# Kernel optimization log

Hardware: AMD Instinct MI355X
Metric: run time of the kernel (lower is better)

Reference implementation:

```python
import jax, jax.numpy as jnp
import numpy as np

H = 16          # num_heads
W = 256         # sliding window size
LN_EPS = 1e-6
ROPE_BASE = 10000.0


def layer_norm(x, g, b):
    m = jnp.mean(x, axis=-1, keepdims=True)
    v = jnp.mean((x - m) ** 2, axis=-1, keepdims=True)
    return (x - m) * jax.lax.rsqrt(v + LN_EPS) * g + b


def rope(x):
    # x: [B, S, H, hd]; rotate-half RoPE
    S, hd = x.shape[1], x.shape[-1]
    inv_freq = 1.0 / (ROPE_BASE ** (jnp.arange(0, hd, 2, dtype=jnp.float32) / hd))
    ang = jnp.arange(S, dtype=jnp.float32)[:, None] * inv_freq[None, :]  # [S, hd/2]
    cos = jnp.concatenate([jnp.cos(ang), jnp.cos(ang)], axis=-1)[None, :, None, :]
    sin = jnp.concatenate([jnp.sin(ang), jnp.sin(ang)], axis=-1)[None, :, None, :]
    x1, x2 = jnp.split(x, 2, axis=-1)
    rot = jnp.concatenate([-x2, x1], axis=-1)
    return x * cos + rot * sin


def setup_inputs() -> dict:
    key = jax.random.key(0)
    ks = jax.random.split(key, 12)
    B, S, D, I = 2, 2048, 1024, 4096
    s = 0.02
    return {
        "hidden_states": jax.random.normal(ks[0], (B, S, D), jnp.float32),
        "wq": jax.random.normal(ks[1], (D, D), jnp.float32) * s,
        "wk": jax.random.normal(ks[2], (D, D), jnp.float32) * s,
        "wv": jax.random.normal(ks[3], (D, D), jnp.float32) * s,
        "wo": jax.random.normal(ks[4], (D, D), jnp.float32) * s,
        "w1": jax.random.normal(ks[5], (D, I), jnp.float32) * s,
        "w2": jax.random.normal(ks[6], (I, D), jnp.float32) * s,
        "w3": jax.random.normal(ks[7], (D, I), jnp.float32) * s,
        "ln1_g": jnp.ones((D,), jnp.float32),
        "ln1_b": jnp.zeros((D,), jnp.float32),
        "ln2_g": jnp.ones((D,), jnp.float32),
        "ln2_b": jnp.zeros((D,), jnp.float32),
    }


def reference(hidden_states, wq, wk, wv, wo, w1, w2, w3, ln1_g, ln1_b, ln2_g, ln2_b):
    B, S, D = hidden_states.shape
    hd = D // H

    # --- attention sub-block ---
    residual = hidden_states
    x = layer_norm(hidden_states, ln1_g, ln1_b)
    q = (x @ wq).reshape(B, S, H, hd)
    k = (x @ wk).reshape(B, S, H, hd)
    v = (x @ wv).reshape(B, S, H, hd)
    q, k = rope(q), rope(k)

    scores = jnp.einsum("bqhd,bkhd->bhqk", q, k) / jnp.sqrt(jnp.float32(hd))
    idx = jnp.arange(S)
    rel = idx[:, None] - idx[None, :]          # i - j
    mask = (rel >= 0) & (rel < W)              # causal sliding window
    scores = jnp.where(mask[None, None], scores, jnp.float32(-1e9))
    attn = jax.nn.softmax(scores, axis=-1)
    ctx = jnp.einsum("bhqk,bkhd->bqhd", attn, v).reshape(B, S, D)
    hidden_states = residual + ctx @ wo

    # --- SwiGLU MLP sub-block ---
    residual = hidden_states
    x = layer_norm(hidden_states, ln2_g, ln2_b)
    mlp = (jax.nn.silu(x @ w1) * (x @ w3)) @ w2
    return residual + mlp
```

## Files before the change

kernel.cpp:

```cpp
#include <hip/hip_runtime.h>
#include <hip/hip_bf16.h>

typedef __bf16 bf16_t;
typedef __bf16 bf16x4 __attribute__((ext_vector_type(4)));
typedef __bf16 bf16x8 __attribute__((ext_vector_type(8)));
typedef float f32x4 __attribute__((ext_vector_type(4)));

#define LN_EPS 1e-6f

__device__ __forceinline__ void gl2lds16(const void* g, void* l) {
    __builtin_amdgcn_global_load_lds(
        (const __attribute__((address_space(1))) void*)g,
        (__attribute__((address_space(3))) void*)l, 16, 0, 0);
}

__device__ __forceinline__ void block_sync() {
    __asm__ __volatile__("" ::: "memory");
    __builtin_amdgcn_s_barrier();
    __asm__ __volatile__("" ::: "memory");
}

__device__ __forceinline__ void ln_row(const float* __restrict__ x, const float* __restrict__ g,
                                       const float* __restrict__ bb, bf16_t* __restrict__ out,
                                       int row, int t, float* sbuf, float* sbuf2) {
    const int D = 1024;
    const float4* xr = reinterpret_cast<const float4*>(x + (size_t)row * D);
    float4 v = xr[t];
    float s = v.x + v.y + v.z + v.w;
    int wave = t >> 6, lane = t & 63;
#pragma unroll
    for (int o = 32; o > 0; o >>= 1) s += __shfl_xor(s, o);
    if (lane == 0) sbuf[wave] = s;
    __syncthreads();
    float mean = (sbuf[0] + sbuf[1] + sbuf[2] + sbuf[3]) / (float)D;
    float d0 = v.x - mean, d1 = v.y - mean, d2 = v.z - mean, d3 = v.w - mean;
    float sq = d0 * d0 + d1 * d1 + d2 * d2 + d3 * d3;
#pragma unroll
    for (int o = 32; o > 0; o >>= 1) sq += __shfl_xor(sq, o);
    if (lane == 0) sbuf2[wave] = sq;
    __syncthreads();
    float var = (sbuf2[0] + sbuf2[1] + sbuf2[2] + sbuf2[3]) / (float)D;
    float inv = rsqrtf(var + LN_EPS);
    float4 gv = reinterpret_cast<const float4*>(g)[t];
    float4 bv = reinterpret_cast<const float4*>(bb)[t];
    bf16x4 o4;
    o4[0] = (bf16_t)(d0 * inv * gv.x + bv.x);
    o4[1] = (bf16_t)(d1 * inv * gv.y + bv.y);
    o4[2] = (bf16_t)(d2 * inv * gv.z + bv.z);
    o4[3] = (bf16_t)(d3 * inv * gv.w + bv.w);
    *reinterpret_cast<bf16x4*>(out + (size_t)row * D + t * 4) = o4;
}

__global__ void prep_weights_kernel(const float* __restrict__ wq, const float* __restrict__ wk,
                                    const float* __restrict__ wv, const float* __restrict__ wo,
                                    const float* __restrict__ w1, const float* __restrict__ w3,
                                    const float* __restrict__ w2, bf16_t* __restrict__ wq_t,
                                    bf16_t* __restrict__ wk_t, bf16_t* __restrict__ wv_t,
                                    bf16_t* __restrict__ wo_t, bf16_t* __restrict__ w13_t,
                                    bf16_t* __restrict__ w2_t, const float* __restrict__ hs,
                                    const float* __restrict__ ln1g, const float* __restrict__ ln1b,
                                    bf16_t* __restrict__ x_b) {
    __shared__ float tile[32][33];
    __shared__ float sbuf[4];
    __shared__ float sbuf2[4];
    int id = blockIdx.x;
    if (id >= 16384) {
        ln_row(hs, ln1g, ln1b, x_b, id - 16384, threadIdx.x, sbuf, sbuf2);
        return;
    }
    const float* src;
    bf16_t* dst;
    int R, C, mode = 0;
    if (id < 4096) {
        int w = id >> 10;
        id &= 1023;
        src = (w == 0) ? wq : (w == 1) ? wk : (w == 2) ? wv : wo;
        dst = (w == 0) ? wq_t : (w == 1) ? wk_t : (w == 2) ? wv_t : wo_t;
        R = 1024; C = 1024;
    } else if (id < 8192) {
        id -= 4096; src = w1; dst = w13_t; R = 1024; C = 4096; mode = 1;
    } else if (id < 12288) {
        id -= 8192; src = w3; dst = w13_t; R = 1024; C = 4096; mode = 2;
    } else {
        id -= 12288; src = w2; dst = w2_t; R = 4096; C = 1024;
    }
    int tpc = C >> 5;
    int bx = id % tpc, by = id / tpc;
    int r0 = by * 32, c0 = bx * 32;
    int tx = threadIdx.x & 31;
    int ty = threadIdx.x >> 5;
#pragma unroll
    for (int i = 0; i < 4; i++) {
        int r = ty + i * 8;
        tile[r][tx] = src[(size_t)(r0 + r) * C + (c0 + tx)];
    }
    __syncthreads();
#pragma unroll
    for (int i = 0; i < 4; i++) {
        int r = ty + i * 8;
        int rr = c0 + r;
        if (mode) rr = ((rr >> 7) << 8) + (rr & 127) + ((mode == 2) ? 128 : 0);
        dst[(size_t)rr * R + (r0 + tx)] = (bf16_t)tile[tx][r];
    }
}

__global__ void ln_kernel(const float* __restrict__ x, const float* __restrict__ g,
                          const float* __restrict__ bb, bf16_t* __restrict__ out, int D) {
    __shared__ float sbuf[4];
    __shared__ float sbuf2[4];
    ln_row(x, g, bb, out, blockIdx.x, threadIdx.x, sbuf, sbuf2);
}

#define G4_BK 64

template <int EPI>
__launch_bounds__(256, 2) __global__
void gemm4_kernel(const bf16_t* __restrict__ A, const bf16_t* __restrict__ Bt,
                  float* __restrict__ Cf, const float* __restrict__ aux,
                  const bf16_t* __restrict__ auxb, bf16_t* __restrict__ Cb,
                  int M, int N, int K, int lda, int ldb) {
    __shared__ __align__(16) bf16_t As[128 * G4_BK];
    __shared__ __align__(16) bf16_t Bs[128 * G4_BK];
    const int t = threadIdx.x;
    const int wave = t >> 6, lane = t & 63;
    const int lr = lane & 15, quad = lane >> 4;
    const int wm = (wave >> 1) * 64, wn = (wave & 1) * 64;

    const int gx = gridDim.x, gy = gridDim.y;
    const int nwg = gx * gy;
    const int lin = blockIdx.y * gx + blockIdx.x;
    const int qch = nwg >> 3;
    const int sw = (lin & 7) * qch + (lin >> 3);
    const int m0 = (sw / gy) * 128;
    const int n0 = (sw % gy) * 128;
    const int koff = blockIdx.z * K;

    const int srow = t >> 3;
    const int sslot = (t & 7) ^ (srow & 7);
    const bf16_t* agp = A + (size_t)(m0 + srow) * lda + koff + sslot * 8;
    const bf16_t* bgp = Bt + (size_t)(n0 + srow) * ldb + koff + sslot * 8;
    bf16_t* asl = As + t * 8;
    bf16_t* bsl = Bs + t * 8;

    int aoff[4][2], boff[4][2];
#pragma unroll
    for (int f = 0; f < 4; f++)
#pragma unroll
        for (int s = 0; s < 2; s++) {
            int ra = wm + f * 16 + lr;
            int rb = wn + f * 16 + lr;
            aoff[f][s] = ra * G4_BK + (((s * 4 + quad) ^ (ra & 7)) << 3);
            boff[f][s] = rb * G4_BK + (((s * 4 + quad) ^ (rb & 7)) << 3);
        }

    f32x4 acc[4][4];
#pragma unroll
    for (int mi = 0; mi < 4; mi++)
#pragma unroll
        for (int ni = 0; ni < 4; ni++) acc[mi][ni] = 0.f;

    for (int k0 = 0; k0 < K; k0 += G4_BK) {
#pragma unroll
        for (int i = 0; i < 4; i++)
            gl2lds16(agp + k0 + (size_t)(32 * i) * lda, asl + i * 2048);
#pragma unroll
        for (int i = 0; i < 4; i++)
            gl2lds16(bgp + k0 + (size_t)(32 * i) * ldb, bsl + i * 2048);
        __syncthreads();
#pragma unroll
        for (int s = 0; s < 2; s++) {
            bf16x8 af[4], bfv[4];
#pragma unroll
            for (int mi = 0; mi < 4; mi++)
                af[mi] = *reinterpret_cast<const bf16x8*>(&As[aoff[mi][s]]);
#pragma unroll
            for (int ni = 0; ni < 4; ni++)
                bfv[ni] = *reinterpret_cast<const bf16x8*>(&Bs[boff[ni][s]]);
#pragma unroll
            for (int mi = 0; mi < 4; mi++)
#pragma unroll
                for (int ni = 0; ni < 4; ni++)
                    acc[mi][ni] = __builtin_amdgcn_mfma_f32_16x16x32_bf16(af[mi], bfv[ni],
                                                                          acc[mi][ni], 0, 0, 0);
        }
        __syncthreads();
    }

#pragma unroll
    for (int mi = 0; mi < 4; mi++)
#pragma unroll
        for (int ni = 0; ni < 4; ni++)
#pragma unroll
            for (int j = 0; j < 4; j++) {
                int gm = m0 + wm + mi * 16 + quad * 4 + j;
                int gn = n0 + wn + ni * 16 + lr;
                size_t idx = (size_t)gm * N + gn;
                float val = acc[mi][ni][j];
                if constexpr (EPI == 1) {
                    Cf[idx] = val + aux[idx];
                }
            }
}


template <int QM, int QN>
__device__ __forceinline__ void quad_mfma(f32x4 (&acc)[2][2][4][2], const bf16x8 (&af)[4][2],
                                          const bf16x8 (&bf)[2][2]) {
#pragma unroll
    for (int fr = 0; fr < 4; fr++)
#pragma unroll
        for (int fc = 0; fc < 2; fc++)
#pragma unroll
            for (int ks = 0; ks < 2; ks++)
                acc[QM][QN][fr][fc] = __builtin_amdgcn_mfma_f32_16x16x32_bf16(
                    af[fr][ks], bf[fc][ks], acc[QM][QN][fr][fc], 0, 0, 0);
}

template <int EPI>
__launch_bounds__(512, 2) __global__
void gemm6_kernel(const bf16_t* __restrict__ A, const bf16_t* __restrict__ Bt,
                  const bf16_t* __restrict__ auxb, bf16_t* __restrict__ Cb,
                  bf16_t* __restrict__ Cb2, int M, int N, int K, int lda, int ldb) {
    extern __shared__ __align__(16) bf16_t smem[];
    bf16_t* smA = smem;
    bf16_t* smB = smem + 32768;
    const int t = threadIdx.x;
    const int wave = t >> 6, lane = t & 63;
    const int lr = lane & 15, quad = lane >> 4;
    const int rowgrp = wave >> 2;
    const int colgrp = wave & 3;
    const int cg1 = colgrp & 1, cg2 = colgrp >> 1;

    const int gx = gridDim.x, gy = gridDim.y;
    const int nwg = gx * gy;
    const int lin = blockIdx.y * gx + blockIdx.x;
    int m0t, n0t;
    if (gy == 32) {
        int s = lin >> 8, r = lin & 255, x = r & 7, j = r >> 3;
        m0t = s * 8 + (x & 1) * 4 + (j >> 3);
        n0t = (x >> 1) * 8 + (j & 7);
    } else if (gy == 12) {
        int x = lin & 7, j = lin >> 3;
        m0t = (x & 3) * 4 + j / 6;
        n0t = (x >> 2) * 6 + j % 6;
    } else {
        const int qch = nwg >> 3;
        const int sw = (lin & 7) * qch + (lin >> 3);
        m0t = sw / gy;
        n0t = sw % gy;
    }
    const int m0 = m0t * 256;
    const int n0 = n0t * 256;
    const int koff = blockIdx.z * K;

    const bf16_t* Ag = A + (size_t)m0 * lda + koff;
    const bf16_t* Bg = Bt + (size_t)n0 * ldb + koff;

    const int li0 = (wave * 2 + 0) * 64 + lane;
    const int li1 = (wave * 2 + 1) * 64 + lane;
    const int r0s = li0 >> 3, c0s = ((li0 & 7) ^ (r0s & 7)) << 3;
    const int r1s = li1 >> 3, c1s = ((li1 & 7) ^ (r1s & 7)) << 3;
    const bf16_t* pA0[2] = {Ag + (size_t)r0s * lda + c0s, Ag + (size_t)r1s * lda + c1s};
    const bf16_t* pA1[2] = {pA0[0] + (size_t)128 * lda, pA0[1] + (size_t)128 * lda};
    const bf16_t* pB0[2] = {Bg + (size_t)r0s * ldb + c0s, Bg + (size_t)r1s * ldb + c1s};
    const bf16_t* pB1[2] = {pB0[0] + (size_t)128 * ldb, pB0[1] + (size_t)128 * ldb};
    const int dl0 = (wave * 2 + 0) * 512;
    const int dl1 = (wave * 2 + 1) * 512;

#define STG(P, LBASE)                          \
    do {                                       \
        gl2lds16(P[0], (LBASE) + dl0);         \
        P[0] += 64;                            \
        gl2lds16(P[1], (LBASE) + dl1);         \
        P[1] += 64;                            \
    } while (0)

    int aoff[4][2], boff[2][2];
#pragma unroll
    for (int fr = 0; fr < 4; fr++)
#pragma unroll
        for (int ks = 0; ks < 2; ks++) {
            int ra = rowgrp * 64 + fr * 16 + lr;
            aoff[fr][ks] = ra * 64 + (((ks * 4 + quad) ^ (ra & 7)) << 3);
        }
#pragma unroll
    for (int fc = 0; fc < 2; fc++)
#pragma unroll
        for (int ks = 0; ks < 2; ks++) {
            int rb = cg1 * 64 + cg2 * 16 + fc * 32 + lr;
            boff[fc][ks] = rb * 64 + (((ks * 4 + quad) ^ (rb & 7)) << 3);
        }

    f32x4 acc[2][2][4][2];
#pragma unroll
    for (int qm = 0; qm < 2; qm++)
#pragma unroll
        for (int qn = 0; qn < 2; qn++)
#pragma unroll
            for (int fr = 0; fr < 4; fr++)
#pragma unroll
                for (int fc = 0; fc < 2; fc++) acc[qm][qn][fr][fc] = 0.f;

    const int NT = K >> 6;

    STG(pA0, smA);
    STG(pB0, smB);
    STG(pB1, smB + 8192);
    STG(pA1, smA + 8192);
    if (NT > 1) {
        STG(pA0, smA + 16384);
        __asm__ __volatile__("s_waitcnt vmcnt(2)" ::: "memory");
    } else {
        __asm__ __volatile__("s_waitcnt vmcnt(0)" ::: "memory");
    }
    block_sync();

    bf16x8 af[4][2], bf0[2][2], bf1[2][2];

    for (int tt = 0; tt < NT; ++tt) {
        const int cur = tt & 1, nxt = cur ^ 1;
        const bf16_t* A0b = smA + cur * 16384;
        const bf16_t* A1b = A0b + 8192;
        const bf16_t* B0b = smB + cur * 16384;
        const bf16_t* B1b = B0b + 8192;
        bf16_t* sAn = smA + nxt * 16384;
        bf16_t* sBn = smB + nxt * 16384;
        bf16_t* sAc = smA + cur * 16384;
        const bool pf1 = (tt + 1 < NT);
        const bool pf2 = (tt + 2 < NT);

#pragma unroll
        for (int fr = 0; fr < 4; fr++)
#pragma unroll
            for (int ks = 0; ks < 2; ks++)
                af[fr][ks] = *reinterpret_cast<const bf16x8*>(A0b + aoff[fr][ks]);
#pragma unroll
        for (int fc = 0; fc < 2; fc++)
#pragma unroll
            for (int ks = 0; ks < 2; ks++)
                bf0[fc][ks] = *reinterpret_cast<const bf16x8*>(B0b + boff[fc][ks]);
        if (pf1) STG(pB0, sBn);
        block_sync();
        __asm__ __volatile__("s_waitcnt lgkmcnt(0)" ::: "memory");
        __builtin_amdgcn_sched_barrier(0);
        __builtin_amdgcn_s_setprio(1);
        quad_mfma<0, 0>(acc, af, bf0);
        __builtin_amdgcn_s_setprio(0);
        block_sync();

#pragma unroll
        for (int fc = 0; fc < 2; fc++)
#pragma unroll
            for (int ks = 0; ks < 2; ks++)
                bf1[fc][ks] = *reinterpret_cast<const bf16x8*>(B1b + boff[fc][ks]);
        if (pf1) STG(pB1, sBn + 8192);
        block_sync();
        __asm__ __volatile__("s_waitcnt lgkmcnt(0)" ::: "memory");
        __builtin_amdgcn_sched_barrier(0);
        __builtin_amdgcn_s_setprio(1);
        quad_mfma<0, 1>(acc, af, bf1);
        __builtin_amdgcn_s_setprio(0);
        block_sync();

#pragma unroll
        for (int fr = 0; fr < 4; fr++)
#pragma unroll
            for (int ks = 0; ks < 2; ks++)
                af[fr][ks] = *reinterpret_cast<const bf16x8*>(A1b + aoff[fr][ks]);
        if (pf1) STG(pA1, sAn + 8192);
        block_sync();
        __asm__ __volatile__("s_waitcnt lgkmcnt(0)" ::: "memory");
        __builtin_amdgcn_sched_barrier(0);
        __builtin_amdgcn_s_setprio(1);
        quad_mfma<1, 1>(acc, af, bf1);
        __builtin_amdgcn_s_setprio(0);
        block_sync();

        if (pf2) STG(pA0, sAc);
        __builtin_amdgcn_s_setprio(1);
        quad_mfma<1, 0>(acc, af, bf0);
        __builtin_amdgcn_s_setprio(0);
        __asm__ __volatile__("s_waitcnt vmcnt(2)" ::: "memory");
        block_sync();
    }
#undef STG

    if constexpr (EPI == 3) {
        if (n0 < 2048) {
            const float kfreq = -0.41524101186f;
            const int d = cg2 * 16 + lr;
            const float freq = exp2f((float)d * kfreq);
#pragma unroll
            for (int qm = 0; qm < 2; qm++)
#pragma unroll
                for (int qn = 0; qn < 2; qn++) {
                    const int gnb = n0 + qn * 128 + cg1 * 64;
#pragma unroll
                    for (int fr = 0; fr < 4; fr++)
#pragma unroll
                        for (int j = 0; j < 4; j++) {
                            int gm = m0 + qm * 128 + rowgrp * 64 + fr * 16 + quad * 4 + j;
                            float pos = (float)(gm & 2047);
                            float ang = pos * freq;
                            float sn, cs;
                            __sincosf(ang, &sn, &cs);
                            float x1 = acc[qm][qn][fr][0][j];
                            float x2 = acc[qm][qn][fr][1][j];
                            size_t idx = (size_t)gm * N + gnb + d;
                            Cb[idx] = (bf16_t)(x1 * cs - x2 * sn);
                            Cb[idx + 32] = (bf16_t)(x2 * cs + x1 * sn);
                        }
                }
        } else {
#pragma unroll
            for (int qm = 0; qm < 2; qm++)
#pragma unroll
                for (int qn = 0; qn < 2; qn++)
#pragma unroll
                    for (int fr = 0; fr < 4; fr++)
#pragma unroll
                        for (int fc = 0; fc < 2; fc++) {
                            int gmb = m0 + qm * 128 + rowgrp * 64 + fr * 16 + quad * 4;
                            int vcol = (n0 - 2048) + qn * 128 + cg1 * 64 + cg2 * 16 + fc * 32 + lr;
                            int hh = vcol >> 6, dd = vcol & 63;
                            int bb2 = gmb >> 11, ss = gmb & 2047;
                            bf16x4 pk;
#pragma unroll
                            for (int j = 0; j < 4; j++) pk[j] = (bf16_t)acc[qm][qn][fr][fc][j];
                            *reinterpret_cast<bf16x4*>(
                                &Cb2[(((size_t)(bb2 * 16 + hh)) * 64 + dd) * 2048 + ss]) = pk;
                        }
        }
    } else if constexpr (EPI == 6) {
        const int No = N >> 1;
#pragma unroll
        for (int qm = 0; qm < 2; qm++)
#pragma unroll
            for (int fr = 0; fr < 4; fr++)
#pragma unroll
                for (int fc = 0; fc < 2; fc++)
#pragma unroll
                    for (int j = 0; j < 4; j++) {
                        int gm = m0 + qm * 128 + rowgrp * 64 + fr * 16 + quad * 4 + j;
                        int c = (n0 >> 1) + cg1 * 64 + cg2 * 16 + fc * 32 + lr;
                        float a = acc[qm][0][fr][fc][j];
                        float bv = acc[qm][1][fr][fc][j];
                        float sl = a / (1.0f + __expf(-a));
                        Cb[(size_t)gm * No + c] = (bf16_t)(sl * bv);
                    }
    } else {
        size_t outoff = (EPI == 5) ? (size_t)blockIdx.z * M * N : 0;
#pragma unroll
        for (int qm = 0; qm < 2; qm++)
#pragma unroll
            for (int qn = 0; qn < 2; qn++)
#pragma unroll
                for (int fr = 0; fr < 4; fr++)
#pragma unroll
                    for (int fc = 0; fc < 2; fc++)
#pragma unroll
                        for (int j = 0; j < 4; j++) {
                            int gm = m0 + qm * 128 + rowgrp * 64 + fr * 16 + quad * 4 + j;
                            int gn = n0 + qn * 128 + cg1 * 64 + cg2 * 16 + fc * 32 + lr;
                            size_t idx = (size_t)gm * N + gn;
                            float val = acc[qm][qn][fr][fc][j];
                            if constexpr (EPI == 5) {
                                Cb[outoff + idx] = (bf16_t)val;
                            } else {
                                Cb[idx] = (bf16_t)val;
                            }
                        }
    }
}

__global__ void reduce4_kernel(const bf16_t* __restrict__ p, const float* __restrict__ hid,
                               float* __restrict__ out, int n4) {
    int i = blockIdx.x * 256 + threadIdx.x;
    if (i >= n4) return;
    size_t i4 = (size_t)i * 4;
    float4 h = *reinterpret_cast<const float4*>(hid + i4);
    const size_t stride = (size_t)4096 * 1024;
#pragma unroll
    for (int c = 0; c < 4; c++) {
        bf16x4 a = *reinterpret_cast<const bf16x4*>(p + c * stride + i4);
        h.x += (float)a[0];
        h.y += (float)a[1];
        h.z += (float)a[2];
        h.w += (float)a[3];
    }
    *reinterpret_cast<float4*>(out + i4) = h;
}

#define PSTR 40
#define QKVS 3072
__global__ __launch_bounds__(256, 2) void attn_kernel(const bf16_t* __restrict__ qkv,
                                                      const bf16_t* __restrict__ vt,
                                                      bf16_t* __restrict__ ctx, int S) {
    __shared__ __align__(16) bf16_t Pbuf[4][16 * PSTR];
    int t = threadIdx.x;
    int wave = t >> 6, lane = t & 63;
    int col = lane & 15, quad = lane >> 4;
    int h = blockIdx.y, b = blockIdx.z;
    int q0 = blockIdx.x * 64 + wave * 16;

    const bf16_t* qrow = qkv + (size_t)(b * S + q0 + col) * QKVS + h * 64;
    bf16x8 aq0 = *reinterpret_cast<const bf16x8*>(qrow + quad * 8);
    bf16x8 aq1 = *reinterpret_cast<const bf16x8*>(qrow + 32 + quad * 8);

    int jbase = q0 - 256;
    f32x4 sc[17];
#pragma unroll
    for (int kt = 0; kt < 17; kt++) {
        int j = jbase + kt * 16 + col;
        int jc = j < 0 ? 0 : (j > S - 1 ? S - 1 : j);
        const bf16_t* krow = qkv + (size_t)(b * S + jc) * QKVS + 1024 + h * 64;
        bf16x8 bk0 = *reinterpret_cast<const bf16x8*>(krow + quad * 8);
        bf16x8 bk1 = *reinterpret_cast<const bf16x8*>(krow + 32 + quad * 8);
        f32x4 c0 = {0.f, 0.f, 0.f, 0.f};
        c0 = __builtin_amdgcn_mfma_f32_16x16x32_bf16(aq0, bk0, c0, 0, 0, 0);
        c0 = __builtin_amdgcn_mfma_f32_16x16x32_bf16(aq1, bk1, c0, 0, 0, 0);
        sc[kt] = c0;
    }
#pragma unroll
    for (int kt = 0; kt < 17; kt++) {
#pragma unroll
        for (int jj = 0; jj < 4; jj++) {
            int qq = quad * 4 + jj;
            int j = jbase + kt * 16 + col;
            int rel = (q0 + qq) - j;
            bool ok = (j >= 0) && (rel >= 0) && (rel < 256);
            sc[kt][jj] = ok ? sc[kt][jj] * 0.125f : -1e30f;
        }
    }
    float sminv[4];
#pragma unroll
    for (int jj = 0; jj < 4; jj++) {
        float m = -1e30f;
#pragma unroll
        for (int kt = 0; kt < 17; kt++) m = fmaxf(m, sc[kt][jj]);
#pragma unroll
        for (int o = 1; o < 16; o <<= 1) m = fmaxf(m, __shfl_xor(m, o));
        float s = 0.f;
#pragma unroll
        for (int kt = 0; kt < 17; kt++) {
            float p = __expf(sc[kt][jj] - m);
            sc[kt][jj] = p;
            s += p;
        }
#pragma unroll
        for (int o = 1; o < 16; o <<= 1) s += __shfl_xor(s, o);
        sminv[jj] = 1.0f / s;
    }
    f32x4 o[4];
#pragma unroll
    for (int n = 0; n < 4; n++) o[n] = 0.f;
    bf16_t* myP = Pbuf[wave];
    const bf16_t* vplane = vt + ((size_t)(b * 16 + h)) * 64 * S;
#pragma unroll
    for (int c = 0; c < 9; c++) {
#pragma unroll
        for (int half = 0; half < 2; half++) {
            int kt = 2 * c + half;
#pragma unroll
            for (int jj = 0; jj < 4; jj++) {
                int qq = quad * 4 + jj;
                bf16_t pv = (kt < 17) ? (bf16_t)(sc[kt < 17 ? kt : 0][jj] * sminv[jj])
                                      : (bf16_t)0.f;
                myP[qq * PSTR + half * 16 + col] = pv;
            }
        }
        bf16x8 ap = *reinterpret_cast<const bf16x8*>(myP + col * PSTR + quad * 8);
        int key0 = jbase + c * 32 + quad * 8;
        int kc = key0 < 0 ? 0 : (key0 > S - 8 ? S - 8 : key0);
#pragma unroll
        for (int n = 0; n < 4; n++) {
            bf16x8 bv = *reinterpret_cast<const bf16x8*>(vplane + ((size_t)(n * 16 + col)) * S + kc);
            o[n] = __builtin_amdgcn_mfma_f32_16x16x32_bf16(ap, bv, o[n], 0, 0, 0);
        }
    }
#pragma unroll
    for (int n = 0; n < 4; n++)
#pragma unroll
        for (int jj = 0; jj < 4; jj++) {
            int qq = quad * 4 + jj;
            ctx[((size_t)(b * S + q0 + qq) * 16 + h) * 64 + n * 16 + col] = (bf16_t)o[n][jj];
        }
}

extern "C" void kernel_launch(void* const* d_in, const int* in_sizes, int n_in,
                              void* d_out, int out_size, void* d_ws, size_t ws_size,
                              hipStream_t stream) {
    const float* hs   = (const float*)d_in[0];
    const float* wq   = (const float*)d_in[1];
    const float* wk   = (const float*)d_in[2];
    const float* wv   = (const float*)d_in[3];
    const float* wo   = (const float*)d_in[4];
    const float* w1   = (const float*)d_in[5];
    const float* w2   = (const float*)d_in[6];
    const float* w3   = (const float*)d_in[7];
    const float* ln1g = (const float*)d_in[8];
    const float* ln1b = (const float*)d_in[9];
    const float* ln2g = (const float*)d_in[10];
    const float* ln2b = (const float*)d_in[11];
    float* out = (float*)d_out;

    const int B = 2, S = 2048, D = 1024, I = 4096;
    const int BS = B * S;

    char* ws = (char*)d_ws;
    const size_t MB = 1024 * 1024;
    bf16_t* wq_t  = (bf16_t*)(ws + 0 * MB);
    bf16_t* wk_t  = (bf16_t*)(ws + 2 * MB);
    bf16_t* wv_t  = (bf16_t*)(ws + 4 * MB);
    bf16_t* wo_t  = (bf16_t*)(ws + 6 * MB);
    bf16_t* w13_t = (bf16_t*)(ws + 8 * MB);
    bf16_t* w2_t  = (bf16_t*)(ws + 24 * MB);
    bf16_t* x_b   = (bf16_t*)(ws + 32 * MB);
    float*  hid   = (float*)(ws + 40 * MB);
    bf16_t* x2_b  = (bf16_t*)(ws + 56 * MB);
    bf16_t* qkvb  = (bf16_t*)(ws + 64 * MB);
    bf16_t* vt    = (bf16_t*)(ws + 88 * MB);
    bf16_t* ctxb  = (bf16_t*)(ws + 96 * MB);
    bf16_t* hbuf  = (bf16_t*)(ws + 96 * MB);
    bf16_t* pker  = (bf16_t*)(ws + 64 * MB);

    hipFuncSetAttribute(reinterpret_cast<const void*>(&gemm6_kernel<3>),
                        hipFuncAttributeMaxDynamicSharedMemorySize, 131072);
    hipFuncSetAttribute(reinterpret_cast<const void*>(&gemm6_kernel<5>),
                        hipFuncAttributeMaxDynamicSharedMemorySize, 131072);
    hipFuncSetAttribute(reinterpret_cast<const void*>(&gemm6_kernel<6>),
                        hipFuncAttributeMaxDynamicSharedMemorySize, 131072);

    dim3 tb(256);
    dim3 tb6(512);

    prep_weights_kernel<<<dim3(20480), tb, 0, stream>>>(wq, wk, wv, wo, w1, w3, w2, wq_t, wk_t,
                                                        wv_t, wo_t, w13_t, w2_t, hs, ln1g, ln1b,
                                                        x_b);

    gemm6_kernel<3><<<dim3(BS / 256, 3072 / 256), tb6, 131072, stream>>>(
        x_b, wq_t, nullptr, qkvb, vt, BS, 3072, D, D, D);

    attn_kernel<<<dim3(S / 64, 16, B), tb, 0, stream>>>(qkvb, vt, ctxb, S);

    gemm4_kernel<1><<<dim3(BS / 128, D / 128), tb, 0, stream>>>(
        ctxb, wo_t, hid, hs, nullptr, nullptr, BS, D, D, D, D);

    ln_kernel<<<BS, tb, 0, stream>>>(hid, ln2g, ln2b, x2_b, D);

    gemm6_kernel<6><<<dim3(BS / 256, 8192 / 256), tb6, 131072, stream>>>(
        x2_b, w13_t, nullptr, hbuf, nullptr, BS, 8192, D, D, D);

    gemm6_kernel<5><<<dim3(BS / 256, D / 256, 4), tb6, 131072, stream>>>(
        hbuf, w2_t, nullptr, pker, nullptr, BS, D, 1024, I, I);
    reduce4_kernel<<<dim3(BS * D / 4 / 256), tb, 0, stream>>>(pker, hid, out, BS * D / 4);
}
```

Before: 340.4 us.

## Use 32x32x16 MFMA tiles in new GEMM kernel for MLP GEMMs

Adds a gemm7 kernel that computes each wave's sub-tile with 32x32x16 bf16 MFMA instructions instead of 16x16 fragments, with new LDS fragment offsets and a matching epilogue register-to-row mapping. The fused SwiGLU up-projection and the split-K down-projection now use this kernel, while the QKV GEMM stays on gemm6. Larger MFMA tiles need fewer LDS fragment reads and MFMA issues per FLOP, which should raise matrix-core throughput. The epilogue now writes scalar bf16 values in a strided pattern, which could hurt store efficiency.

```diff
diff --git a/kernel.cpp b/kernel.cpp
--- a/kernel.cpp
+++ b/kernel.cpp
@@ -5,6 +5,7 @@
 typedef __bf16 bf16x4 __attribute__((ext_vector_type(4)));
 typedef __bf16 bf16x8 __attribute__((ext_vector_type(8)));
 typedef float f32x4 __attribute__((ext_vector_type(4)));
+typedef float f32x16 __attribute__((ext_vector_type(16)));
 
 #define LN_EPS 1e-6f
 
@@ -235,11 +236,7 @@
     const int nwg = gx * gy;
     const int lin = blockIdx.y * gx + blockIdx.x;
     int m0t, n0t;
-    if (gy == 32) {
-        int s = lin >> 8, r = lin & 255, x = r & 7, j = r >> 3;
-        m0t = s * 8 + (x & 1) * 4 + (j >> 3);
-        n0t = (x >> 1) * 8 + (j & 7);
-    } else if (gy == 12) {
+    if (gy == 12) {
         int x = lin & 7, j = lin >> 3;
         m0t = (x & 3) * 4 + j / 6;
         n0t = (x >> 2) * 6 + j % 6;
@@ -431,45 +428,208 @@
                                 &Cb2[(((size_t)(bb2 * 16 + hh)) * 64 + dd) * 2048 + ss]) = pk;
                         }
         }
-    } else if constexpr (EPI == 6) {
+    }
+}
+
+
+template <int QM, int QN>
+__device__ __forceinline__ void quad_mfma32(f32x16 (&acc)[2][2][2], const bf16x8 (&af)[2][4],
+                                            const bf16x8 (&bf)[4]) {
+#pragma unroll
+    for (int ks = 0; ks < 4; ks++)
+#pragma unroll
+        for (int mf = 0; mf < 2; mf++)
+            acc[QM][QN][mf] = __builtin_amdgcn_mfma_f32_32x32x16_bf16(
+                af[mf][ks], bf[ks], acc[QM][QN][mf], 0, 0, 0);
+}
+
+template <int EPI>
+__launch_bounds__(512, 2) __global__
+void gemm7_kernel(const bf16_t* __restrict__ A, const bf16_t* __restrict__ Bt,
+                  bf16_t* __restrict__ Cb, int M, int N, int K, int lda, int ldb) {
+    extern __shared__ __align__(16) bf16_t smem[];
+    bf16_t* smA = smem;
+    bf16_t* smB = smem + 32768;
+    const int t = threadIdx.x;
+    const int wave = t >> 6, lane = t & 63;
+    const int l31 = lane & 31, lh = lane >> 5;
+    const int rowgrp = wave >> 2;
+    const int wn = wave & 3;
+
+    const int gx = gridDim.x, gy = gridDim.y;
+    const int nwg = gx * gy;
+    const int lin = blockIdx.y * gx + blockIdx.x;
+    int m0t, n0t;
+    if (gy == 32) {
+        int s = lin >> 8, r = lin & 255, x = r & 7, j = r >> 3;
+        m0t = s * 8 + (x & 1) * 4 + (j >> 3);
+        n0t = (x >> 1) * 8 + (j & 7);
+    } else {
+        const int qch = nwg >> 3;
+        const int sw = (lin & 7) * qch + (lin >> 3);
+        m0t = sw / gy;
+        n0t = sw % gy;
+    }
+    const int m0 = m0t * 256;
+    const int n0 = n0t * 256;
+    const int koff = blockIdx.z * K;
+
+    const bf16_t* Ag = A + (size_t)m0 * lda + koff;
+    const bf16_t* Bg = Bt + (size_t)n0 * ldb + koff;
+
+    const int li0 = (wave * 2 + 0) * 64 + lane;
+    const int li1 = (wave * 2 + 1) * 64 + lane;
+    const int r0s = li0 >> 3, c0s = ((li0 & 7) ^ (r0s & 7)) << 3;
+    const int r1s = li1 >> 3, c1s = ((li1 & 7) ^ (r1s & 7)) << 3;
+    const bf16_t* pA0[2] = {Ag + (size_t)r0s * lda + c0s, Ag + (size_t)r1s * lda + c1s};
+    const bf16_t* pA1[2] = {pA0[0] + (size_t)128 * lda, pA0[1] + (size_t)128 * lda};
+    const bf16_t* pB0[2] = {Bg + (size_t)r0s * ldb + c0s, Bg + (size_t)r1s * ldb + c1s};
+    const bf16_t* pB1[2] = {pB0[0] + (size_t)128 * ldb, pB0[1] + (size_t)128 * ldb};
+    const int dl0 = (wave * 2 + 0) * 512;
+    const int dl1 = (wave * 2 + 1) * 512;
+
+#define STG(P, LBASE)                          \
+    do {                                       \
+        gl2lds16(P[0], (LBASE) + dl0);         \
+        P[0] += 64;                            \
+        gl2lds16(P[1], (LBASE) + dl1);         \
+        P[1] += 64;                            \
+    } while (0)
+
+    int aoff[2][4], boff[4];
+#pragma unroll
+    for (int mf = 0; mf < 2; mf++)
+#pragma unroll
+        for (int ks = 0; ks < 4; ks++) {
+            int ra = rowgrp * 64 + mf * 32 + l31;
+            aoff[mf][ks] = ra * 64 + (((ks * 2 + lh) ^ (ra & 7)) << 3);
+        }
+#pragma unroll
+    for (int ks = 0; ks < 4; ks++) {
+        int rb = wn * 32 + l31;
+        boff[ks] = rb * 64 + (((ks * 2 + lh) ^ (rb & 7)) << 3);
+    }
+
+    f32x16 acc[2][2][2];
+#pragma unroll
+    for (int qm = 0; qm < 2; qm++)
+#pragma unroll
+        for (int qn = 0; qn < 2; qn++)
+#pragma unroll
+            for (int mf = 0; mf < 2; mf++) acc[qm][qn][mf] = 0.f;
+
+    const int NT = K >> 6;
+
+    STG(pA0, smA);
+    STG(pB0, smB);
+    STG(pB1, smB + 8192);
+    STG(pA1, smA + 8192);
+    if (NT > 1) {
+        STG(pA0, smA + 16384);
+        __asm__ __volatile__("s_waitcnt vmcnt(2)" ::: "memory");
+    } else {
+        __asm__ __volatile__("s_waitcnt vmcnt(0)" ::: "memory");
+    }
+    block_sync();
+
+    bf16x8 af[2][4], bf0[4], bf1[4];
+
+    for (int tt = 0; tt < NT; ++tt) {
+        const int cur = tt & 1, nxt = cur ^ 1;
+        const bf16_t* A0b = smA + cur * 16384;
+        const bf16_t* A1b = A0b + 8192;
+        const bf16_t* B0b = smB + cur * 16384;
+        const bf16_t* B1b = B0b + 8192;
+        bf16_t* sAn = smA + nxt * 16384;
+        bf16_t* sBn = smB + nxt * 16384;
+        bf16_t* sAc = smA + cur * 16384;
+        const bool pf1 = (tt + 1 < NT);
+        const bool pf2 = (tt + 2 < NT);
+
+#pragma unroll
+        for (int mf = 0; mf < 2; mf++)
+#pragma unroll
+            for (int ks = 0; ks < 4; ks++)
+                af[mf][ks] = *reinterpret_cast<const bf16x8*>(A0b + aoff[mf][ks]);
+#pragma unroll
+        for (int ks = 0; ks < 4; ks++)
+            bf0[ks] = *reinterpret_cast<const bf16x8*>(B0b + boff[ks]);
+        if (pf1) STG(pB0, sBn);
+        block_sync();
+        __asm__ __volatile__("s_waitcnt lgkmcnt(0)" ::: "memory");
+        __builtin_amdgcn_sched_barrier(0);
+        __builtin_amdgcn_s_setprio(1);
+        quad_mfma32<0, 0>(acc, af, bf0);
+        __builtin_amdgcn_s_setprio(0);
+        block_sync();
+
+#pragma unroll
+        for (int ks = 0; ks < 4; ks++)
+            bf1[ks] = *reinterpret_cast<const bf16x8*>(B1b + boff[ks]);
+        if (pf1) STG(pB1, sBn + 8192);
+        block_sync();
+        __asm__ __volatile__("s_waitcnt lgkmcnt(0)" ::: "memory");
+        __builtin_amdgcn_sched_barrier(0);
+        __builtin_amdgcn_s_setprio(1);
+        quad_mfma32<0, 1>(acc, af, bf1);
+        __builtin_amdgcn_s_setprio(0);
+        block_sync();
+
+#pragma unroll
+        for (int mf = 0; mf < 2; mf++)
+#pragma unroll
+            for (int ks = 0; ks < 4; ks++)
+                af[mf][ks] = *reinterpret_cast<const bf16x8*>(A1b + aoff[mf][ks]);
+        if (pf1) STG(pA1, sAn + 8192);
+        block_sync();
+        __asm__ __volatile__("s_waitcnt lgkmcnt(0)" ::: "memory");
+        __builtin_amdgcn_sched_barrier(0);
+        __builtin_amdgcn_s_setprio(1);
+        quad_mfma32<1, 1>(acc, af, bf1);
+        __builtin_amdgcn_s_setprio(0);
+        block_sync();
+
+        if (pf2) STG(pA0, sAc);
+        __builtin_amdgcn_s_setprio(1);
+        quad_mfma32<1, 0>(acc, af, bf0);
+        __builtin_amdgcn_s_setprio(0);
+        __asm__ __volatile__("s_waitcnt vmcnt(2)" ::: "memory");
+        block_sync();
+    }
+#undef STG
+
+    if constexpr (EPI == 6) {
         const int No = N >> 1;
+        const int c = (n0 >> 1) + wn * 32 + l31;
 #pragma unroll
         for (int qm = 0; qm < 2; qm++)
 #pragma unroll
-            for (int fr = 0; fr < 4; fr++)
-#pragma unroll
-                for (int fc = 0; fc < 2; fc++)
-#pragma unroll
-                    for (int j = 0; j < 4; j++) {
-                        int gm = m0 + qm * 128 + rowgrp * 64 + fr * 16 + quad * 4 + j;
-                        int c = (n0 >> 1) + cg1 * 64 + cg2 * 16 + fc * 32 + lr;
-                        float a = acc[qm][0][fr][fc][j];
-                        float bv = acc[qm][1][fr][fc][j];
-                        float sl = a / (1.0f + __expf(-a));
-                        Cb[(size_t)gm * No + c] = (bf16_t)(sl * bv);
-                    }
+            for (int mf = 0; mf < 2; mf++)
+#pragma unroll
+                for (int reg = 0; reg < 16; reg++) {
+                    int rrow = (reg & 3) + 8 * (reg >> 2) + 4 * lh;
+                    int gm = m0 + qm * 128 + rowgrp * 64 + mf * 32 + rrow;
+                    float a = acc[qm][0][mf][reg];
+                    float bv = acc[qm][1][mf][reg];
+                    float sl = a / (1.0f + __expf(-a));
+                    Cb[(size_t)gm * No + c] = (bf16_t)(sl * bv);
+                }
     } else {
         size_t outoff = (EPI == 5) ? (size_t)blockIdx.z * M * N : 0;
 #pragma unroll
         for (int qm = 0; qm < 2; qm++)
 #pragma unroll
-            for (int qn = 0; qn < 2; qn++)
-#pragma unroll
-                for (int fr = 0; fr < 4; fr++)
-#pragma unroll
-                    for (int fc = 0; fc < 2; fc++)
-#pragma unroll
-                        for (int j = 0; j < 4; j++) {
-                            int gm = m0 + qm * 128 + rowgrp * 64 + fr * 16 + quad * 4 + j;
-                            int gn = n0 + qn * 128 + cg1 * 64 + cg2 * 16 + fc * 32 + lr;
-                            size_t idx = (size_t)gm * N + gn;
-                            float val = acc[qm][qn][fr][fc][j];
-                            if constexpr (EPI == 5) {
-                                Cb[outoff + idx] = (bf16_t)val;
-                            } else {
-                                Cb[idx] = (bf16_t)val;
-                            }
-                        }
+            for (int qn = 0; qn < 2; qn++) {
+                const int gn = n0 + qn * 128 + wn * 32 + l31;
+#pragma unroll
+                for (int mf = 0; mf < 2; mf++)
+#pragma unroll
+                    for (int reg = 0; reg < 16; reg++) {
+                        int rrow = (reg & 3) + 8 * (reg >> 2) + 4 * lh;
+                        int gm = m0 + qm * 128 + rowgrp * 64 + mf * 32 + rrow;
+                        Cb[outoff + (size_t)gm * N + gn] = (bf16_t)acc[qm][qn][mf][reg];
+                    }
+            }
     }
 }
 
@@ -626,9 +786,9 @@
 
     hipFuncSetAttribute(reinterpret_cast<const void*>(&gemm6_kernel<3>),
                         hipFuncAttributeMaxDynamicSharedMemorySize, 131072);
-    hipFuncSetAttribute(reinterpret_cast<const void*>(&gemm6_kernel<5>),
+    hipFuncSetAttribute(reinterpret_cast<const void*>(&gemm7_kernel<5>),
                         hipFuncAttributeMaxDynamicSharedMemorySize, 131072);
-    hipFuncSetAttribute(reinterpret_cast<const void*>(&gemm6_kernel<6>),
+    hipFuncSetAttribute(reinterpret_cast<const void*>(&gemm7_kernel<6>),
                         hipFuncAttributeMaxDynamicSharedMemorySize, 131072);
 
     dim3 tb(256);
@@ -648,10 +808,10 @@
 
     ln_kernel<<<BS, tb, 0, stream>>>(hid, ln2g, ln2b, x2_b, D);
 
-    gemm6_kernel<6><<<dim3(BS / 256, 8192 / 256), tb6, 131072, stream>>>(
-        x2_b, w13_t, nullptr, hbuf, nullptr, BS, 8192, D, D, D);
-
-    gemm6_kernel<5><<<dim3(BS / 256, D / 256, 4), tb6, 131072, stream>>>(
-        hbuf, w2_t, nullptr, pker, nullptr, BS, D, 1024, I, I);
+    gemm7_kernel<6><<<dim3(BS / 256, 8192 / 256), tb6, 131072, stream>>>(
+        x2_b, w13_t, hbuf, BS, 8192, D, D, D);
+
+    gemm7_kernel<5><<<dim3(BS / 256, D / 256, 4), tb6, 131072, stream>>>(
+        hbuf, w2_t, pker, BS, D, 1024, I, I);
     reduce4_kernel<<<dim3(BS * D / 4 / 256), tb, 0, stream>>>(pker, hid, out, BS * D / 4);
 }
```

Result: slower. 352.2 us (+3.5%).

## Replace split-K down projection with single gemm4 pass fusing residual add

Applied to the files above, without the earlier changes.

The MLP down projection no longer runs as a four-way split-K 256x256 gemm writing bf16 partials followed by a separate reduction kernel. It now uses the 128x128 gemm4 kernel over the full K=4096, with the residual added in its epilogue. This removes the partial-buffer traffic and one launch, but gives up the extra parallelism from splitting K (256 blocks instead of 512 waves of work). It also adds s_setprio around the MFMA groups in the attention kernel to favour issuing matrix instructions.

```diff
diff --git a/kernel.cpp b/kernel.cpp
--- a/kernel.cpp
+++ b/kernel.cpp
@@ -448,47 +448,7 @@
                         float sl = a / (1.0f + __expf(-a));
                         Cb[(size_t)gm * No + c] = (bf16_t)(sl * bv);
                     }
-    } else {
-        size_t outoff = (EPI == 5) ? (size_t)blockIdx.z * M * N : 0;
-#pragma unroll
-        for (int qm = 0; qm < 2; qm++)
-#pragma unroll
-            for (int qn = 0; qn < 2; qn++)
-#pragma unroll
-                for (int fr = 0; fr < 4; fr++)
-#pragma unroll
-                    for (int fc = 0; fc < 2; fc++)
-#pragma unroll
-                        for (int j = 0; j < 4; j++) {
-                            int gm = m0 + qm * 128 + rowgrp * 64 + fr * 16 + quad * 4 + j;
-                            int gn = n0 + qn * 128 + cg1 * 64 + cg2 * 16 + fc * 32 + lr;
-                            size_t idx = (size_t)gm * N + gn;
-                            float val = acc[qm][qn][fr][fc][j];
-                            if constexpr (EPI == 5) {
-                                Cb[outoff + idx] = (bf16_t)val;
-                            } else {
-                                Cb[idx] = (bf16_t)val;
-                            }
-                        }
-    }
-}
-
-__global__ void reduce4_kernel(const bf16_t* __restrict__ p, const float* __restrict__ hid,
-                               float* __restrict__ out, int n4) {
-    int i = blockIdx.x * 256 + threadIdx.x;
-    if (i >= n4) return;
-    size_t i4 = (size_t)i * 4;
-    float4 h = *reinterpret_cast<const float4*>(hid + i4);
-    const size_t stride = (size_t)4096 * 1024;
-#pragma unroll
-    for (int c = 0; c < 4; c++) {
-        bf16x4 a = *reinterpret_cast<const bf16x4*>(p + c * stride + i4);
-        h.x += (float)a[0];
-        h.y += (float)a[1];
-        h.z += (float)a[2];
-        h.w += (float)a[3];
-    }
-    *reinterpret_cast<float4*>(out + i4) = h;
+    }
 }
 
 #define PSTR 40
@@ -517,8 +477,10 @@
         bf16x8 bk0 = *reinterpret_cast<const bf16x8*>(krow + quad * 8);
         bf16x8 bk1 = *reinterpret_cast<const bf16x8*>(krow + 32 + quad * 8);
         f32x4 c0 = {0.f, 0.f, 0.f, 0.f};
+        __builtin_amdgcn_s_setprio(1);
         c0 = __builtin_amdgcn_mfma_f32_16x16x32_bf16(aq0, bk0, c0, 0, 0, 0);
         c0 = __builtin_amdgcn_mfma_f32_16x16x32_bf16(aq1, bk1, c0, 0, 0, 0);
+        __builtin_amdgcn_s_setprio(0);
         sc[kt] = c0;
     }
 #pragma unroll
@@ -572,11 +534,13 @@
         bf16x8 ap = *reinterpret_cast<const bf16x8*>(myP + col * PSTR + quad * 8);
         int key0 = jbase + c * 32 + quad * 8;
         int kc = key0 < 0 ? 0 : (key0 > S - 8 ? S - 8 : key0);
+        __builtin_amdgcn_s_setprio(1);
 #pragma unroll
         for (int n = 0; n < 4; n++) {
             bf16x8 bv = *reinterpret_cast<const bf16x8*>(vplane + ((size_t)(n * 16 + col)) * S + kc);
             o[n] = __builtin_amdgcn_mfma_f32_16x16x32_bf16(ap, bv, o[n], 0, 0, 0);
         }
+        __builtin_amdgcn_s_setprio(0);
     }
 #pragma unroll
     for (int n = 0; n < 4; n++)
@@ -622,11 +586,8 @@
     bf16_t* vt    = (bf16_t*)(ws + 88 * MB);
     bf16_t* ctxb  = (bf16_t*)(ws + 96 * MB);
     bf16_t* hbuf  = (bf16_t*)(ws + 96 * MB);
-    bf16_t* pker  = (bf16_t*)(ws + 64 * MB);
 
     hipFuncSetAttribute(reinterpret_cast<const void*>(&gemm6_kernel<3>),
-                        hipFuncAttributeMaxDynamicSharedMemorySize, 131072);
-    hipFuncSetAttribute(reinterpret_cast<const void*>(&gemm6_kernel<5>),
                         hipFuncAttributeMaxDynamicSharedMemorySize, 131072);
     hipFuncSetAttribute(reinterpret_cast<const void*>(&gemm6_kernel<6>),
                         hipFuncAttributeMaxDynamicSharedMemorySize, 131072);
@@ -651,7 +612,6 @@
     gemm6_kernel<6><<<dim3(BS / 256, 8192 / 256), tb6, 131072, stream>>>(
         x2_b, w13_t, nullptr, hbuf, nullptr, BS, 8192, D, D, D);
 
-    gemm6_kernel<5><<<dim3(BS / 256, D / 256, 4), tb6, 131072, stream>>>(
-        hbuf, w2_t, nullptr, pker, nullptr, BS, D, 1024, I, I);
-    reduce4_kernel<<<dim3(BS * D / 4 / 256), tb, 0, stream>>>(pker, hid, out, BS * D / 4);
-}
+    gemm4_kernel<1><<<dim3(BS / 128, D / 128), tb, 0, stream>>>(
+        hbuf, w2_t, out, hid, nullptr, nullptr, BS, D, I, I, I);
+}
```

After: 373.5 us. 9.7% more time.
